# Kernel tuning notes

Measured on AMD Instinct MI355X. Metric: run time of the kernel, lower is better.

## Reference

```python
import jax, jax.numpy as jnp
import numpy as np

J_THR = 0.5
E_THR = 0.5
STRIDE = 4.0
N_LAYERS = 3
NFEAT = 256
SCORER_HIDDEN = 128


def setup_inputs() -> dict:
    key = jax.random.key(0)
    ks = jax.random.split(key, 8)
    B, C, h, w = 4, NFEAT, 128, 128
    inp = {
        "j_logits": jax.random.normal(ks[0], (B, 1, h, w), dtype=jnp.float32),
        "offsets": jax.random.uniform(ks[1], (B, 2, h, w), dtype=jnp.float32),
        "node_feats_map": jax.random.normal(ks[2], (B, C, h, w), dtype=jnp.float32) * 0.1,
        "W_self": jax.random.normal(ks[3], (N_LAYERS, C, C), dtype=jnp.float32) / np.sqrt(C).astype(np.float32),
        "W_nbr": jax.random.normal(ks[4], (N_LAYERS, C, C), dtype=jnp.float32) / np.sqrt(C).astype(np.float32),
        "b_gnn": jnp.zeros((N_LAYERS, C), dtype=jnp.float32),
        "Ws1": jax.random.normal(ks[5], (2 * C, SCORER_HIDDEN), dtype=jnp.float32) / np.sqrt(2.0 * C).astype(np.float32),
        "bs1": jnp.zeros((SCORER_HIDDEN,), dtype=jnp.float32),
        "Ws2": jax.random.normal(ks[6], (SCORER_HIDDEN,), dtype=jnp.float32) / np.sqrt(SCORER_HIDDEN).astype(np.float32),
        "bs2": jnp.zeros((), dtype=jnp.float32),
        "max_nodes": 256,
    }
    return inp


def _complete_graph(n):
    # src repeats node i (n-1) times; dst enumerates all j != i, matching torch complete_graph
    src = np.repeat(np.arange(n), n - 1)
    grid = np.tile(np.arange(n), (n, 1))
    dst = grid[~np.eye(n, dtype=bool)]
    return jnp.asarray(src, dtype=jnp.int32), jnp.asarray(dst, dtype=jnp.int32)


def reference(j_logits, offsets, node_feats_map, W_self, W_nbr, b_gnn, Ws1, bs1, Ws2, bs2, max_nodes):
    B, _, h, w = j_logits.shape
    C = node_feats_map.shape[1]
    N = int(max_nodes)
    src, dst = _complete_graph(N)  # [E], E = N*(N-1)

    def per_image(jl, off, nmap):
        prob = jax.nn.sigmoid(jl[0].reshape(-1))            # [h*w]
        topv, topi = jax.lax.top_k(prob, N)                  # fixed-size stream compaction
        valid = topv > J_THR                                 # [N] mask replacing dynamic nonzero
        iy = topi // w
        ix = topi % w
        yo = off[0].reshape(-1)[topi]
        xo = off[1].reshape(-1)[topi]
        xs = (ix.astype(jnp.float32) + 0.5 + xo) * STRIDE
        ys = (iy.astype(jnp.float32) + 0.5 + yo) * STRIDE
        nodes = jnp.stack([xs, ys], axis=-1)                 # [N,2]
        x = nmap.reshape(C, -1)[:, topi].T * valid[:, None].astype(nmap.dtype)  # [N,C]
        ev = (valid[src] & valid[dst]).astype(x.dtype)       # [E] edge validity
        deg = jax.ops.segment_sum(ev, dst, num_segments=N)   # [N]
        inv_deg = jnp.where(deg > 0, 1.0 / jnp.maximum(deg, 1.0), 0.0)
        for l in range(W_self.shape[0]):
            msg = x[src] * ev[:, None]                       # gather + mask [E,C]
            agg = jax.ops.segment_sum(msg, dst, num_segments=N) * inv_deg[:, None]
            x = jax.nn.relu(x @ W_self[l] + agg @ W_nbr[l] + b_gnn[l]) * valid[:, None].astype(x.dtype)
        hcat = jnp.concatenate([x[src], x[dst]], axis=-1)    # [E,2C]
        hid = jax.nn.relu(hcat @ Ws1 + bs1)                  # [E,H]
        logits = hid @ Ws2 + bs2                             # [E]
        probs = jax.nn.sigmoid(logits)
        keep = (probs > E_THR) & (ev > 0)
        return nodes, x, logits, keep

    nodes, node_emb, edge_logits, keep = jax.vmap(per_image)(j_logits, offsets, node_feats_map)
    return nodes, node_emb, edge_logits, keep
```

## Files before the change

kernel.cpp:

```cpp
#include <hip/hip_runtime.h>

#define NPIX 16384
#define NN   256
#define CC   256
#define HH   128
#define EE   65280
#define BB   4
#define NG   8

typedef __attribute__((ext_vector_type(8))) short short8;
typedef __attribute__((ext_vector_type(4))) float f32x4;

__device__ __forceinline__ unsigned short f2bf(float f){
  unsigned b = __float_as_uint(f);
  return (unsigned short)((b + 0x7fffu + ((b >> 16) & 1u)) >> 16);
}
__device__ __forceinline__ float bf2f(unsigned short s){ return __uint_as_float(((unsigned)s) << 16); }

__global__ __launch_bounds__(256) void k_conv(
    const float* __restrict__ Wself, const float* __restrict__ Wnbr,
    const float* __restrict__ Ws1,
    unsigned short* __restrict__ wbfT, unsigned short* __restrict__ wuvT)
{
  __shared__ float tile[32][33];
  const int blk = blockIdx.x;
  const int m = blk >> 6;
  const int t = blk & 63;
  const int r4 = threadIdx.x >> 5;
  const int cl = threadIdx.x & 31;
  if (m < 6) {
    const int tr = t >> 3, tc = t & 7;
    const float* src = (m < 3) ? (Wself + (size_t)m*65536) : (Wnbr + (size_t)(m-3)*65536);
    unsigned short* dT = wbfT + (size_t)m*65536;
    #pragma unroll
    for (int rr = 0; rr < 4; ++rr) {
      int r = r4*4 + rr;
      tile[r][cl] = src[(size_t)(tr*32 + r)*256 + tc*32 + cl];
    }
    __syncthreads();
    #pragma unroll
    for (int rr = 0; rr < 4; ++rr) {
      int r = r4*4 + rr;
      dT[(size_t)(tc*32 + r)*256 + tr*32 + cl] = f2bf(tile[cl][r]);
    }
  } else {
    const int tr = t >> 2, tc = t & 3;
    #pragma unroll
    for (int rr = 0; rr < 4; ++rr) {
      int r = r4*4 + rr;
      tile[r][cl] = Ws1[(size_t)(tr*32 + r)*128 + tc*32 + cl];
    }
    __syncthreads();
    #pragma unroll
    for (int rr = 0; rr < 4; ++rr) {
      int r = r4*4 + rr;
      int h  = tc*32 + r;
      int cg = tr*32 + cl;
      int col = h + ((cg >= 256) ? 128 : 0);
      wuvT[(size_t)col*256 + (cg & 255)] = f2bf(tile[cl][r]);
    }
  }
}

__global__ __launch_bounds__(1024) void k_topk(
    const float* __restrict__ jl, const float* __restrict__ off,
    int* __restrict__ topi, int* __restrict__ valid, float* __restrict__ inv_deg,
    float* __restrict__ out_nodes, float* __restrict__ Sbuf)
{
  __shared__ int hist[NG][257];
  __shared__ int histT[256];
  __shared__ unsigned long long s_sel[NN];
  __shared__ unsigned long long s_T;
  __shared__ int s_digit, s_krem, s_cnt, s_vcnt, s_break;

  const int b = blockIdx.x;
  const int tid = threadIdx.x;
  const int grp = (tid >> 7) & (NG - 1);
  if (tid == 0) { s_cnt = 0; s_vcnt = 0; }

  {
    int l = tid >> 8, c = tid & 255;
    Sbuf[l*BB*CC + b*CC + c] = 0.0f;
  }

  unsigned long long rk[16];
  const float* p = jl + (size_t)b * NPIX;
  #pragma unroll
  for (int r = 0; r < 16; ++r) {
    int i = tid + (r << 10);
    float x = p[i];
    float pr = 1.0f / (1.0f + expf(-x));
    unsigned bits = __float_as_uint(pr);
    rk[r] = ((unsigned long long)bits << 32) | (unsigned)(0xFFFFFFFFu - (unsigned)i);
  }

  unsigned long long prefix = 0;
  int k = NN;
  int shift = 56;
  int brk = 0;
  for (int pass = 0; pass < 8 && !brk; ++pass) {
    shift = 56 - 8 * pass;
    for (int i = tid; i < NG * 257; i += 1024) ((int*)hist)[i] = 0;
    __syncthreads();
    unsigned long long pmask = (pass == 0) ? 0ULL : (~0ULL << (shift + 8));
    #pragma unroll
    for (int r = 0; r < 16; ++r) {
      unsigned long long kk = rk[r];
      if ((kk & pmask) == prefix)
        atomicAdd(&hist[grp][(int)((kk >> shift) & 255)], 1);
    }
    __syncthreads();
    if (tid < 256) {
      int t = 0;
      #pragma unroll
      for (int g = 0; g < NG; ++g) t += hist[g][tid];
      histT[tid] = t;
    }
    __syncthreads();
    if (tid < 64) {
      int h0 = histT[4*tid + 0], h1 = histT[4*tid + 1];
      int h2 = histT[4*tid + 2], h3 = histT[4*tid + 3];
      int tot = h0 + h1 + h2 + h3;
      int suf = tot;
      #pragma unroll
      for (int d = 1; d < 64; d <<= 1) {
        int o = __shfl_down(suf, d);
        if (tid + d < 64) suf += o;
      }
      int above = suf - tot;
      int c3 = h3 + above;
      int c2 = c3 + h2;
      int c1 = c2 + h1;
      int c0 = c1 + h0;
      if      (c3 >= k && above < k) { s_digit = 4*tid+3; s_krem = k - above; s_break = (h3 == 1); }
      else if (c2 >= k && c3    < k) { s_digit = 4*tid+2; s_krem = k - c3;    s_break = (h2 == 1); }
      else if (c1 >= k && c2    < k) { s_digit = 4*tid+1; s_krem = k - c2;    s_break = (h1 == 1); }
      else if (c0 >= k && c1    < k) { s_digit = 4*tid+0; s_krem = k - c1;    s_break = (h0 == 1); }
    }
    __syncthreads();
    prefix |= ((unsigned long long)s_digit) << shift;
    k = s_krem;
    brk = s_break;
  }

  if (shift == 0) {
    if (tid == 0) s_T = prefix;
  } else {
    unsigned long long known_mask = ~0ULL << shift;
    #pragma unroll
    for (int r = 0; r < 16; ++r)
      if ((rk[r] & known_mask) == prefix) s_T = rk[r];
  }
  __syncthreads();
  unsigned long long T = s_T;

  #pragma unroll
  for (int r = 0; r < 16; ++r) {
    unsigned long long kk = rk[r];
    if (kk >= T) { int pos = atomicAdd(&s_cnt, 1); s_sel[pos] = kk; }
  }
  __syncthreads();

  int my_rank = -1, my_v = 0;
  if (tid < NN) {
    unsigned long long mine = s_sel[tid];
    int rank = 0;
    #pragma unroll 16
    for (int j = 0; j < NN; ++j) rank += (s_sel[j] > mine) ? 1 : 0;
    unsigned bits = (unsigned)(mine >> 32);
    int v = bits > 0x3F000000u ? 1 : 0;
    int idx = (int)(0xFFFFFFFFu - (unsigned)(mine & 0xFFFFFFFFull));
    if (v) atomicAdd(&s_vcnt, 1);
    topi[b*NN + rank] = idx;
    valid[b*NN + rank] = v;
    int iy = idx >> 7;
    int ix = idx & 127;
    float yo = off[((size_t)b*2 + 0) * NPIX + idx];
    float xo = off[((size_t)b*2 + 1) * NPIX + idx];
    out_nodes[(b*NN + rank)*2 + 0] = ((float)ix + 0.5f + xo) * 4.0f;
    out_nodes[(b*NN + rank)*2 + 1] = ((float)iy + 0.5f + yo) * 4.0f;
    my_rank = rank; my_v = v;
  }
  __syncthreads();
  if (tid < NN) {
    int V = s_vcnt;
    inv_deg[b*NN + my_rank] = (my_v && V >= 2) ? 1.0f / (float)(V - 1) : 0.0f;
  }
}

__global__ __launch_bounds__(256) void k_gather(
    const float* __restrict__ nmap, const int* __restrict__ topi,
    const int* __restrict__ valid, unsigned short* __restrict__ x, float* __restrict__ S0)
{
  const int bn = blockIdx.x;
  const int b = bn >> 8;
  const int c = threadIdx.x;
  int pix = topi[bn];
  int v = valid[bn];
  float val = v ? nmap[(((size_t)b*CC + c) << 14) + pix] : 0.0f;
  unsigned short hb = f2bf(val);
  x[(size_t)bn*CC + c] = hb;
  float valr = bf2f(hb);
  if (valr != 0.0f) atomicAdd(&S0[b*CC + c], valr);
}

__global__ __launch_bounds__(256) void k_gnn(
    const unsigned short* __restrict__ x, const float* __restrict__ S,
    const float* __restrict__ inv_deg, const int* __restrict__ valid,
    const unsigned short* __restrict__ wT1, const unsigned short* __restrict__ wT2,
    const float* __restrict__ bias, unsigned short* __restrict__ xout,
    float* __restrict__ Snext,
    float* __restrict__ out_emb)
{
  __shared__ float sA1[16][33];
  __shared__ float sA2[16][33];
  __shared__ float sP2p[8][33];
  __shared__ float sP2[32];
  const int mt = blockIdx.x >> 3;
  const int cg = blockIdx.x & 7;
  const int row0 = mt * 16;
  const int b = row0 >> 8;
  const int tid = threadIdx.x;
  const int wave = tid >> 6;
  const int lane = tid & 63;

  {
    const int cl = tid >> 3;
    const int kw = tid & 7;
    const unsigned short* wrow = wT2 + (size_t)(cg*32 + cl)*256 + kw*32;
    const float* Sb = S + b*CC + kw*32;
    float a = 0.f;
    #pragma unroll 8
    for (int i = 0; i < 32; ++i) a += Sb[i] * bf2f(wrow[i]);
    sP2p[kw][cl] = a;
  }
  __syncthreads();
  if (tid < 32) {
    float s = 0.f;
    #pragma unroll
    for (int g = 0; g < 8; ++g) s += sP2p[g][tid];
    sP2[tid] = s;
  }

  const unsigned short* wT = (wave < 2) ? wT1 : wT2;
  const int colbase = cg*32 + (wave & 1)*16;
  const int arow = row0 + (lane & 15);
  const int koff = (lane >> 4) * 8;

  const short8* aptr = (const short8*)(x + (size_t)arow*256 + koff);
  const short8* bptr = (const short8*)(wT + (size_t)(colbase + (lane & 15))*256 + koff);

  f32x4 acc = {0.f, 0.f, 0.f, 0.f};
  #pragma unroll
  for (int kk = 0; kk < 8; ++kk) {
    short8 af = aptr[kk*4];
    short8 bf = bptr[kk*4];
    acc = __builtin_amdgcn_mfma_f32_16x16x32_bf16(af, bf, acc, 0, 0, 0);
  }

  {
    float* dst = (wave < 2) ? &sA1[0][0] : &sA2[0][0];
    int ccol = (wave & 1)*16 + (lane & 15);
    #pragma unroll
    for (int r = 0; r < 4; ++r) {
      int crow = (lane >> 4)*4 + r;
      dst[crow*33 + ccol] = acc[r];
    }
  }
  __syncthreads();

  const int row = tid >> 4;
  const int cp2 = tid & 15;
  const int gr = row0 + row;
  const int c0 = cg*32 + 2*cp2;
  float inv = inv_deg[gr];
  int   va  = valid[gr];
  float a10 = sA1[row][2*cp2], a11 = sA1[row][2*cp2+1];
  float a20 = sA2[row][2*cp2], a21 = sA2[row][2*cp2+1];
  float p0 = sP2[2*cp2], p1 = sP2[2*cp2+1];
  float o0 = fmaxf(a10 + inv*(p0 - a20) + bias[c0],     0.f); o0 = va ? o0 : 0.f;
  float o1 = fmaxf(a11 + inv*(p1 - a21) + bias[c0 + 1], 0.f); o1 = va ? o1 : 0.f;

  unsigned short h0 = f2bf(o0), h1 = f2bf(o1);
  ((unsigned*)xout)[(size_t)gr*128 + (cg*16 + cp2)] = (unsigned)h0 | ((unsigned)h1 << 16);
  if (out_emb) {
    float2 v; v.x = o0; v.y = o1;
    *(float2*)&out_emb[(size_t)gr*CC + c0] = v;
  }
  if (Snext) {
    __syncthreads();
    sA1[row][2*cp2]   = bf2f(h0);
    sA1[row][2*cp2+1] = bf2f(h1);
    __syncthreads();
    if (tid < 32) {
      float s = 0.f;
      #pragma unroll
      for (int r = 0; r < 16; ++r) s += sA1[r][tid];
      if (s != 0.f) atomicAdd(&Snext[b*CC + cg*32 + tid], s);
    }
  }
}

__global__ __launch_bounds__(256) void k_uv(
    const unsigned short* __restrict__ x, const unsigned short* __restrict__ wuvT,
    float* __restrict__ u, float* __restrict__ vt)
{
  const int mt = blockIdx.x >> 2;
  const int cg = blockIdx.x & 3;
  const int row0 = mt * 16;
  const int b = row0 >> 8;
  const int wave = threadIdx.x >> 6;
  const int lane = threadIdx.x & 63;
  const int col = cg*64 + wave*16 + (lane & 15);
  const int arow = row0 + (lane & 15);
  const int koff = (lane >> 4) * 8;
  const short8* aptr = (const short8*)(x + (size_t)arow*256 + koff);
  const short8* bptr = (const short8*)(wuvT + (size_t)col*256 + koff);
  f32x4 acc = {0.f, 0.f, 0.f, 0.f};
  #pragma unroll
  for (int kk = 0; kk < 8; ++kk)
    acc = __builtin_amdgcn_mfma_f32_16x16x32_bf16(aptr[kk*4], bptr[kk*4], acc, 0, 0, 0);
  const int rbase = row0 + (lane >> 4)*4;
  if (col < HH) {
    #pragma unroll
    for (int r = 0; r < 4; ++r)
      u[(size_t)(rbase + r)*HH + col] = acc[r];
  } else {
    float4 v; v.x = acc[0]; v.y = acc[1]; v.z = acc[2]; v.w = acc[3];
    *(float4*)&vt[(size_t)(b*HH + (col - HH))*NN + rbase] = v;
  }
}

__global__ __launch_bounds__(256) void k_edges(
    const float* __restrict__ u, const float* __restrict__ vt,
    const float* __restrict__ bs1, const float* __restrict__ Ws2,
    const float* __restrict__ bs2, const int* __restrict__ valid,
    float* __restrict__ out_logits, float* __restrict__ out_keep)
{
  const int b = blockIdx.x >> 8;
  const int i = blockIdx.x & 255;
  const int j = threadIdx.x;
  const float4* u4  = (const float4*)(u + ((size_t)(b*NN + i))*HH);
  const float4* b14 = (const float4*)bs1;
  const float4* w24 = (const float4*)Ws2;
  const float* vrow = vt + (size_t)b*HH*NN;
  float acc = 0.f;
  #pragma unroll 4
  for (int h4 = 0; h4 < 32; ++h4) {
    float4 uu = u4[h4];
    float4 bb = b14[h4];
    float4 ww = w24[h4];
    int hb = h4 << 2;
    float t0 = uu.x + bb.x + vrow[(size_t)(hb+0)*NN + j];
    float t1 = uu.y + bb.y + vrow[(size_t)(hb+1)*NN + j];
    float t2 = uu.z + bb.z + vrow[(size_t)(hb+2)*NN + j];
    float t3 = uu.w + bb.w + vrow[(size_t)(hb+3)*NN + j];
    acc += fmaxf(t0, 0.f)*ww.x + fmaxf(t1, 0.f)*ww.y
         + fmaxf(t2, 0.f)*ww.z + fmaxf(t3, 0.f)*ww.w;
  }
  acc += bs2[0];
  if (j != i) {
    int e = i*255 + (j < i ? j : j - 1);
    int ev = valid[b*NN + i] & valid[b*NN + j];
    out_logits[(size_t)b*EE + e] = acc;
    out_keep  [(size_t)b*EE + e] = (acc > 0.f && ev) ? 1.0f : 0.0f;
  }
}

extern "C" void kernel_launch(void* const* d_in, const int* in_sizes, int n_in,
                              void* d_out, int out_size, void* d_ws, size_t ws_size,
                              hipStream_t stream) {
  const float* jl    = (const float*)d_in[0];
  const float* off   = (const float*)d_in[1];
  const float* nmap  = (const float*)d_in[2];
  const float* Wself = (const float*)d_in[3];
  const float* Wnbr  = (const float*)d_in[4];
  const float* bg    = (const float*)d_in[5];
  const float* Ws1   = (const float*)d_in[6];
  const float* bs1   = (const float*)d_in[7];
  const float* Ws2   = (const float*)d_in[8];
  const float* bs2   = (const float*)d_in[9];

  char* ws = (char*)d_ws;
  int*   topi    = (int*)  (ws + 0);
  int*   valid   = (int*)  (ws + 4096);
  float* inv_deg = (float*)(ws + 8192);
  float* Sbuf    = (float*)(ws + 12288);
  unsigned short* xa = (unsigned short*)(ws + 28672);
  unsigned short* xb = (unsigned short*)(ws + 552960);
  float* u       = (float*)(ws + 1077248);
  float* vt      = (float*)(ws + 1601536);
  unsigned short* wbfT = (unsigned short*)(ws + 2125824);
  unsigned short* wuvT = (unsigned short*)(ws + 2912256);

  float* out        = (float*)d_out;
  float* out_nodes  = out;
  float* out_emb    = out + 2048;
  float* out_logits = out + 264192;
  float* out_keep   = out + 525312;

  hipLaunchKernelGGL(k_conv,   dim3(448),   dim3(256),  0, stream,
                     Wself, Wnbr, Ws1, wbfT, wuvT);
  hipLaunchKernelGGL(k_topk,   dim3(BB),    dim3(1024), 0, stream,
                     jl, off, topi, valid, inv_deg, out_nodes, Sbuf);
  hipLaunchKernelGGL(k_gather, dim3(BB*NN), dim3(256),  0, stream,
                     nmap, topi, valid, xa, Sbuf);

  unsigned short* xc = xa; unsigned short* xn = xb;
  for (int l = 0; l < 3; ++l) {
    hipLaunchKernelGGL(k_gnn, dim3(512), dim3(256),  0, stream,
                       xc, Sbuf + l*BB*CC, inv_deg, valid,
                       wbfT + (size_t)l*65536, wbfT + (size_t)(3 + l)*65536, bg + l*CC,
                       xn,
                       (l < 2) ? (Sbuf + (l+1)*BB*CC) : (float*)nullptr,
                       (l == 2) ? out_emb : (float*)nullptr);
    unsigned short* t = xc; xc = xn; xn = t;
  }

  hipLaunchKernelGGL(k_uv,    dim3(256),   dim3(256), 0, stream, xc, wuvT, u, vt);
  hipLaunchKernelGGL(k_edges, dim3(BB*NN), dim3(256), 0, stream,
                     u, vt, bs1, Ws2, bs2, valid, out_logits, out_keep);
}
```

Before: 81.60 us.

## Merge weight conversion into top-k launch, fold bias into u, restructure edge scorer

```diff
diff --git a/kernel.cpp b/kernel.cpp
--- a/kernel.cpp
+++ b/kernel.cpp
@@ -6,7 +6,7 @@
 #define HH   128
 #define EE   65280
 #define BB   4
-#define NG   8
+#define NG   16
 
 typedef __attribute__((ext_vector_type(8))) short short8;
 typedef __attribute__((ext_vector_type(4))) float f32x4;
@@ -17,65 +17,50 @@
 }
 __device__ __forceinline__ float bf2f(unsigned short s){ return __uint_as_float(((unsigned)s) << 16); }
 
-__global__ __launch_bounds__(256) void k_conv(
+__global__ __launch_bounds__(1024) void k_topk(
+    const float* __restrict__ jl, const float* __restrict__ off,
+    int* __restrict__ topi, int* __restrict__ valid, float* __restrict__ inv_deg,
+    float* __restrict__ out_nodes, float* __restrict__ Sbuf,
     const float* __restrict__ Wself, const float* __restrict__ Wnbr,
     const float* __restrict__ Ws1,
     unsigned short* __restrict__ wbfT, unsigned short* __restrict__ wuvT)
-{
-  __shared__ float tile[32][33];
-  const int blk = blockIdx.x;
-  const int m = blk >> 6;
-  const int t = blk & 63;
-  const int r4 = threadIdx.x >> 5;
-  const int cl = threadIdx.x & 31;
-  if (m < 6) {
-    const int tr = t >> 3, tc = t & 7;
-    const float* src = (m < 3) ? (Wself + (size_t)m*65536) : (Wnbr + (size_t)(m-3)*65536);
-    unsigned short* dT = wbfT + (size_t)m*65536;
-    #pragma unroll
-    for (int rr = 0; rr < 4; ++rr) {
-      int r = r4*4 + rr;
-      tile[r][cl] = src[(size_t)(tr*32 + r)*256 + tc*32 + cl];
-    }
-    __syncthreads();
-    #pragma unroll
-    for (int rr = 0; rr < 4; ++rr) {
-      int r = r4*4 + rr;
-      dT[(size_t)(tc*32 + r)*256 + tr*32 + cl] = f2bf(tile[cl][r]);
-    }
-  } else {
-    const int tr = t >> 2, tc = t & 3;
-    #pragma unroll
-    for (int rr = 0; rr < 4; ++rr) {
-      int r = r4*4 + rr;
-      tile[r][cl] = Ws1[(size_t)(tr*32 + r)*128 + tc*32 + cl];
-    }
-    __syncthreads();
-    #pragma unroll
-    for (int rr = 0; rr < 4; ++rr) {
-      int r = r4*4 + rr;
-      int h  = tc*32 + r;
-      int cg = tr*32 + cl;
-      int col = h + ((cg >= 256) ? 128 : 0);
-      wuvT[(size_t)col*256 + (cg & 255)] = f2bf(tile[cl][r]);
-    }
-  }
-}
-
-__global__ __launch_bounds__(1024) void k_topk(
-    const float* __restrict__ jl, const float* __restrict__ off,
-    int* __restrict__ topi, int* __restrict__ valid, float* __restrict__ inv_deg,
-    float* __restrict__ out_nodes, float* __restrict__ Sbuf)
 {
   __shared__ int hist[NG][257];
   __shared__ int histT[256];
   __shared__ unsigned long long s_sel[NN];
   __shared__ unsigned long long s_T;
   __shared__ int s_digit, s_krem, s_cnt, s_vcnt, s_break;
-
-  const int b = blockIdx.x;
+  __shared__ float tile[32][33];
+
+  const int bid = blockIdx.x;
   const int tid = threadIdx.x;
-  const int grp = (tid >> 7) & (NG - 1);
+
+  if (bid >= BB) {
+    const int blk = bid - BB;
+    const int m = blk >> 6;
+    const int t = blk & 63;
+    const int r  = tid >> 5;
+    const int cl = tid & 31;
+    if (m < 6) {
+      const int tr = t >> 3, tc = t & 7;
+      const float* src = (m < 3) ? (Wself + (size_t)m*65536) : (Wnbr + (size_t)(m-3)*65536);
+      tile[r][cl] = src[(size_t)(tr*32 + r)*256 + tc*32 + cl];
+      __syncthreads();
+      wbfT[(size_t)m*65536 + (size_t)(tc*32 + r)*256 + tr*32 + cl] = f2bf(tile[cl][r]);
+    } else {
+      const int tr = t >> 2, tc = t & 3;
+      tile[r][cl] = Ws1[(size_t)(tr*32 + r)*128 + tc*32 + cl];
+      __syncthreads();
+      int h  = tc*32 + r;
+      int cg = tr*32 + cl;
+      int col = h + ((cg >= 256) ? 128 : 0);
+      wuvT[(size_t)col*256 + (cg & 255)] = f2bf(tile[cl][r]);
+    }
+    return;
+  }
+
+  const int b = bid;
+  const int grp = tid >> 6;
   if (tid == 0) { s_cnt = 0; s_vcnt = 0; }
 
   {
@@ -303,6 +288,7 @@
 
 __global__ __launch_bounds__(256) void k_uv(
     const unsigned short* __restrict__ x, const unsigned short* __restrict__ wuvT,
+    const float* __restrict__ bs1,
     float* __restrict__ u, float* __restrict__ vt)
 {
   const int mt = blockIdx.x >> 2;
@@ -322,9 +308,10 @@
     acc = __builtin_amdgcn_mfma_f32_16x16x32_bf16(aptr[kk*4], bptr[kk*4], acc, 0, 0, 0);
   const int rbase = row0 + (lane >> 4)*4;
   if (col < HH) {
+    float bv = bs1[col];
     #pragma unroll
     for (int r = 0; r < 4; ++r)
-      u[(size_t)(rbase + r)*HH + col] = acc[r];
+      u[(size_t)(rbase + r)*HH + col] = acc[r] + bv;
   } else {
     float4 v; v.x = acc[0]; v.y = acc[1]; v.z = acc[2]; v.w = acc[3];
     *(float4*)&vt[(size_t)(b*HH + (col - HH))*NN + rbase] = v;
@@ -333,37 +320,66 @@
 
 __global__ __launch_bounds__(256) void k_edges(
     const float* __restrict__ u, const float* __restrict__ vt,
-    const float* __restrict__ bs1, const float* __restrict__ Ws2,
-    const float* __restrict__ bs2, const int* __restrict__ valid,
+    const float* __restrict__ Ws2, const float* __restrict__ bs2,
+    const int* __restrict__ valid,
     float* __restrict__ out_logits, float* __restrict__ out_keep)
 {
+  __shared__ float4 red[3][64];
   const int b = blockIdx.x >> 8;
   const int i = blockIdx.x & 255;
-  const int j = threadIdx.x;
-  const float4* u4  = (const float4*)(u + ((size_t)(b*NN + i))*HH);
-  const float4* b14 = (const float4*)bs1;
-  const float4* w24 = (const float4*)Ws2;
-  const float* vrow = vt + (size_t)b*HH*NN;
-  float acc = 0.f;
-  #pragma unroll 4
-  for (int h4 = 0; h4 < 32; ++h4) {
-    float4 uu = u4[h4];
-    float4 bb = b14[h4];
-    float4 ww = w24[h4];
-    int hb = h4 << 2;
-    float t0 = uu.x + bb.x + vrow[(size_t)(hb+0)*NN + j];
-    float t1 = uu.y + bb.y + vrow[(size_t)(hb+1)*NN + j];
-    float t2 = uu.z + bb.z + vrow[(size_t)(hb+2)*NN + j];
-    float t3 = uu.w + bb.w + vrow[(size_t)(hb+3)*NN + j];
-    acc += fmaxf(t0, 0.f)*ww.x + fmaxf(t1, 0.f)*ww.y
-         + fmaxf(t2, 0.f)*ww.z + fmaxf(t3, 0.f)*ww.w;
-  }
-  acc += bs2[0];
-  if (j != i) {
-    int e = i*255 + (j < i ? j : j - 1);
-    int ev = valid[b*NN + i] & valid[b*NN + j];
-    out_logits[(size_t)b*EE + e] = acc;
-    out_keep  [(size_t)b*EE + e] = (acc > 0.f && ev) ? 1.0f : 0.0f;
+  const int tid = threadIdx.x;
+  const int jq = tid & 63;
+  const int kh = tid >> 6;
+  const float* urow = u + ((size_t)(b*NN + i))*HH + kh*32;
+  const float* wrow = Ws2 + kh*32;
+  const float4* vbase = (const float4*)(vt + (size_t)(b*HH + kh*32)*NN) + jq;
+  float ax = 0.f, ay = 0.f, az = 0.f, aw = 0.f;
+  #pragma unroll 8
+  for (int h = 0; h < 32; ++h) {
+    float uh = urow[h];
+    float wh = wrow[h];
+    float4 v = vbase[(size_t)h*64];
+    ax += fmaxf(uh + v.x, 0.f)*wh;
+    ay += fmaxf(uh + v.y, 0.f)*wh;
+    az += fmaxf(uh + v.z, 0.f)*wh;
+    aw += fmaxf(uh + v.w, 0.f)*wh;
+  }
+  if (kh > 0) {
+    float4 t; t.x = ax; t.y = ay; t.z = az; t.w = aw;
+    red[kh-1][jq] = t;
+  }
+  __syncthreads();
+  if (kh == 0) {
+    float4 r0 = red[0][jq], r1 = red[1][jq], r2 = red[2][jq];
+    float bs = bs2[0];
+    float lg0 = ax + r0.x + r1.x + r2.x + bs;
+    float lg1 = ay + r0.y + r1.y + r2.y + bs;
+    float lg2 = az + r0.z + r1.z + r2.z + bs;
+    float lg3 = aw + r0.w + r1.w + r2.w + bs;
+    int vi = valid[b*NN + i];
+    float* Lb = out_logits + (size_t)b*EE;
+    float* Kb = out_keep   + (size_t)b*EE;
+    int j0 = 4*jq;
+    {
+      int j = j0;
+      if (j != i) { int e = i*255 + (j < i ? j : j-1);
+        Lb[e] = lg0; Kb[e] = (lg0 > 0.f && vi && valid[b*NN + j]) ? 1.0f : 0.0f; }
+    }
+    {
+      int j = j0 + 1;
+      if (j != i) { int e = i*255 + (j < i ? j : j-1);
+        Lb[e] = lg1; Kb[e] = (lg1 > 0.f && vi && valid[b*NN + j]) ? 1.0f : 0.0f; }
+    }
+    {
+      int j = j0 + 2;
+      if (j != i) { int e = i*255 + (j < i ? j : j-1);
+        Lb[e] = lg2; Kb[e] = (lg2 > 0.f && vi && valid[b*NN + j]) ? 1.0f : 0.0f; }
+    }
+    {
+      int j = j0 + 3;
+      if (j != i) { int e = i*255 + (j < i ? j : j-1);
+        Lb[e] = lg3; Kb[e] = (lg3 > 0.f && vi && valid[b*NN + j]) ? 1.0f : 0.0f; }
+    }
   }
 }
 
@@ -399,11 +415,10 @@
   float* out_logits = out + 264192;
   float* out_keep   = out + 525312;
 
-  hipLaunchKernelGGL(k_conv,   dim3(448),   dim3(256),  0, stream,
+  hipLaunchKernelGGL(k_topk,   dim3(BB + 448), dim3(1024), 0, stream,
+                     jl, off, topi, valid, inv_deg, out_nodes, Sbuf,
                      Wself, Wnbr, Ws1, wbfT, wuvT);
-  hipLaunchKernelGGL(k_topk,   dim3(BB),    dim3(1024), 0, stream,
-                     jl, off, topi, valid, inv_deg, out_nodes, Sbuf);
-  hipLaunchKernelGGL(k_gather, dim3(BB*NN), dim3(256),  0, stream,
+  hipLaunchKernelGGL(k_gather, dim3(BB*NN),    dim3(256),  0, stream,
                      nmap, topi, valid, xa, Sbuf);
 
   unsigned short* xc = xa; unsigned short* xn = xb;
@@ -417,7 +432,7 @@
     unsigned short* t = xc; xc = xn; xn = t;
   }
 
-  hipLaunchKernelGGL(k_uv,    dim3(256),   dim3(256), 0, stream, xc, wuvT, u, vt);
+  hipLaunchKernelGGL(k_uv,    dim3(256),   dim3(256), 0, stream, xc, wuvT, bs1, u, vt);
   hipLaunchKernelGGL(k_edges, dim3(BB*NN), dim3(256), 0, stream,
-                     u, vt, bs1, Ws2, bs2, valid, out_logits, out_keep);
-}
+                     u, vt, Ws2, bs2, valid, out_logits, out_keep);
+}
```

After: 77.87 us. 4.6% less time.
